# Optimization experiments

Measured on AMD Instinct MI355X. Metric: run time of the kernel, lower is better.

## Reference

```python
import jax, jax.numpy as jnp
import numpy as np
from jax.scipy.ndimage import map_coordinates

B, G, C, H, W = 8, 16, 1, 384, 384
K = 3                    # rectangular (box) kernel size
KV = float(K * K)        # kernel volume (sum of ones kernel)
LBD = 1.0
SMOOTH_DR = 1e-5         # monai LNCC default smooth_dr (smooth_nr = 0)


def setup_inputs() -> dict:
    key = jax.random.key(0)
    k1, k2 = jax.random.split(key)
    images = jax.random.normal(k1, (B, G, C, H, W), dtype=jnp.float32)
    warps = jax.random.normal(k2, (B, G, 2, H, W), dtype=jnp.float32)
    return {"images": images, "warps": warps}


def _warp2d(images, flow):
    """Bilinear warp. images [N,C,H,W], flow [N,2,H,W] (pixel displacements,
    channel 0 = x/width, channel 1 = y/height). Border-clamped sampling."""
    gy, gx = jnp.meshgrid(jnp.arange(H, dtype=images.dtype),
                          jnp.arange(W, dtype=images.dtype), indexing="ij")
    cy = gy[None] + flow[:, 1]   # [N,H,W]
    cx = gx[None] + flow[:, 0]   # [N,H,W]

    def samp(img2d, cy_, cx_):
        return map_coordinates(img2d, [cy_, cx_], order=1, mode="nearest")

    # vmap over channels, then over batch
    per_img = jax.vmap(samp, in_axes=(0, None, None))        # over C
    return jax.vmap(per_img, in_axes=(0, 0, 0))(images, cy, cx)  # over N


def _box_sum(x):
    """3x3 box-filter sum with zero padding (SAME). x: [N,C,H,W]."""
    k = jnp.ones((1, 1, K, K), x.dtype)
    return jax.lax.conv_general_dilated(
        x, k, window_strides=(1, 1), padding="SAME",
        dimension_numbers=("NCHW", "OIHW", "NCHW"))


def _lncc_loss(pred, target):
    """monai LocalNormalizedCrossCorrelationLoss (rectangular kernel)."""
    t_sum = _box_sum(target)
    p_sum = _box_sum(pred)
    t2_sum = _box_sum(target * target)
    p2_sum = _box_sum(pred * pred)
    tp_sum = _box_sum(target * pred)
    t_avg = t_sum / KV
    p_avg = p_sum / KV
    cross = tp_sum - p_avg * t_sum
    t_var = jnp.maximum(t2_sum - t_avg * t_sum, 0.0)
    p_var = jnp.maximum(p2_sum - p_avg * p_sum, 0.0)
    ncc = (cross * cross) / (t_var * p_var + SMOOTH_DR)
    return -jnp.mean(ncc)


def reference(images, warps):
    imgs = images.reshape(B * G, C, H, W)
    flow = warps.reshape(B * G, 2, H, W)
    warped = _warp2d(imgs, flow)                       # [B*G,C,H,W]
    template = jnp.mean(warped, axis=0, keepdims=True)  # [1,C,H,W]
    lncc = _lncc_loss(jnp.broadcast_to(template, warped.shape), warped)
    # Grad2d('l2') on warps [B,G,2,H,W]
    dy = warps[:, :, :, 1:, :] - warps[:, :, :, :-1, :]
    dx = warps[:, :, :, :, 1:] - warps[:, :, :, :, :-1]
    g2 = (jnp.mean(dx * dx) + jnp.mean(dy * dy)) / 2.0
    return lncc + LBD * g2
```

## Files before the change

### kernel.cpp

```cpp
#include <hip/hip_runtime.h>
#include <hip/hip_fp16.h>

#define HH 384
#define WW 384
#define HW (HH * WW)
#define NIMG 128
#define NPIX (NIMG * HW)
#define GRAD_CNT 37650432.0

#define K1_TH 8
#define K1_M  3
#define K1_NT (HH / K1_TH)
#define K1_SROWS (K1_TH + 2 * K1_M)
#define K1_LS 428
#define NP_G (K1_NT * NIMG)

#define K2_SPLIT 4

#define K3_T 32
#define K3_NX (WW / K3_T)
#define K3_TILES (K3_NX * (HH / K3_T))
#define NP_N (K3_TILES * NIMG)

__device__ inline int skew_off(int x) {
    int g = x >> 2;
    return 4 * (g + (g >> 3)) + (x & 3);
}

__device__ inline void block_reduce_store_256(float v, float* dst) {
    #pragma unroll
    for (int o = 32; o > 0; o >>= 1) v += __shfl_down(v, o);
    __shared__ float s[4];
    int wave = threadIdx.x >> 6, lane = threadIdx.x & 63;
    if (lane == 0) s[wave] = v;
    __syncthreads();
    if (threadIdx.x == 0) *dst = s[0] + s[1] + s[2] + s[3];
}

__global__ __launch_bounds__(256, 6) void warp_grad_kernel(
        const float* __restrict__ images, const float* __restrict__ warps,
        __half* __restrict__ warped, float* __restrict__ partialsG) {
    __shared__ float simg[K1_SROWS * K1_LS];
    int n = blockIdx.y;
    int yt = blockIdx.x;
    int y0 = yt * K1_TH;
    int ys0 = max(0, y0 - K1_M);
    int ys1 = min(HH - 1, y0 + K1_TH - 1 + K1_M);
    int cnt = ys1 - ys0 + 1;
    const float* img = images + (size_t)n * HW;
    int tid = threadIdx.x;

    for (int i = tid; i < cnt * 96; i += 256) {
        int r = i / 96, gg = i - r * 96;
        float4 v = *(const float4*)(img + (ys0 + r) * WW + gg * 4);
        *(float4*)(simg + r * K1_LS + 4 * (gg + (gg >> 3))) = v;
    }
    __syncthreads();

    const float* flow0 = warps + (size_t)n * 2 * HW;
    const float* flow1 = flow0 + HW;
    float g = 0.f;

    #pragma unroll
    for (int gi = 0; gi < 3; ++gi) {
        int p4 = gi * 256 + tid;
        int r = p4 / 96;
        int c4 = p4 - r * 96;
        int x0 = c4 * 4;
        int y = y0 + r;
        int base = y * WW + x0;

        float4 f0 = *(const float4*)(flow0 + base);
        float4 f1 = *(const float4*)(flow1 + base);

        float d;
        d = f0.y - f0.x; g += d * d;  d = f1.y - f1.x; g += d * d;
        d = f0.z - f0.y; g += d * d;  d = f1.z - f1.y; g += d * d;
        d = f0.w - f0.z; g += d * d;  d = f1.w - f1.z; g += d * d;
        if (x0 + 4 < WW) {
            float a0 = flow0[base + 4], a1 = flow1[base + 4];
            d = a0 - f0.w; g += d * d;  d = a1 - f1.w; g += d * d;
        }
        if (y + 1 < HH) {
            float4 b0 = *(const float4*)(flow0 + base + WW);
            float4 b1 = *(const float4*)(flow1 + base + WW);
            d = b0.x - f0.x; g += d * d;  d = b1.x - f1.x; g += d * d;
            d = b0.y - f0.y; g += d * d;  d = b1.y - f1.y; g += d * d;
            d = b0.z - f0.z; g += d * d;  d = b1.z - f1.z; g += d * d;
            d = b0.w - f0.w; g += d * d;  d = b1.w - f1.w; g += d * d;
        }

        float fxa[4] = {f0.x, f0.y, f0.z, f0.w};
        float fya[4] = {f1.x, f1.y, f1.z, f1.w};
        float o[4];
        #pragma unroll
        for (int j = 0; j < 4; ++j) {
            float cx = (float)(x0 + j) + fxa[j];
            float cy = (float)y + fya[j];
            float flx = floorf(cx), fly = floorf(cy);
            float wx = cx - flx, wy = cy - fly;
            int xi = (int)flx, yi = (int)fly;
            int x0c = min(max(xi, 0), WW - 1), x1c = min(max(xi + 1, 0), WW - 1);
            int y0c = min(max(yi, 0), HH - 1), y1c = min(max(yi + 1, 0), HH - 1);
            float v00, v01, v10, v11;
            if (y0c >= ys0 && y1c <= ys1) {
                const float* r0 = simg + (y0c - ys0) * K1_LS;
                const float* r1 = simg + (y1c - ys0) * K1_LS;
                int oa = skew_off(x0c), ob = skew_off(x1c);
                v00 = r0[oa]; v01 = r0[ob];
                v10 = r1[oa]; v11 = r1[ob];
            } else {
                v00 = img[y0c * WW + x0c]; v01 = img[y0c * WW + x1c];
                v10 = img[y1c * WW + x0c]; v11 = img[y1c * WW + x1c];
            }
            float top = v00 + wx * (v01 - v00);
            float bot = v10 + wx * (v11 - v10);
            o[j] = top + wy * (bot - top);
        }
        union { __half2 h2[2]; uint2 u; } cv;
        cv.h2[0] = __floats2half2_rn(o[0], o[1]);
        cv.h2[1] = __floats2half2_rn(o[2], o[3]);
        *(uint2*)(warped + (size_t)n * HW + base) = cv.u;
    }
    block_reduce_store_256(g, &partialsG[(size_t)n * K1_NT + yt]);
}

__global__ __launch_bounds__(256) void template_part_kernel(
        const __half* __restrict__ warped, float* __restrict__ tpart) {
    int p4 = blockIdx.x * 256 + threadIdx.x;
    int q = blockIdx.y;
    const __half* p = warped + (size_t)q * (NIMG / K2_SPLIT) * HW + p4 * 4;
    float4 s = {0.f, 0.f, 0.f, 0.f};
    #pragma unroll 8
    for (int nn = 0; nn < NIMG / K2_SPLIT; ++nn) {
        union { uint2 u; __half2 h2[2]; } cv;
        cv.u = *(const uint2*)(p + (size_t)nn * HW);
        float2 lo = __half22float2(cv.h2[0]);
        float2 hi = __half22float2(cv.h2[1]);
        s.x += lo.x; s.y += lo.y; s.z += hi.x; s.w += hi.y;
    }
    *(float4*)(tpart + (size_t)q * HW + p4 * 4) = s;
}

__global__ __launch_bounds__(256) void lncc_kernel(
        const __half* __restrict__ warped, const float* __restrict__ tpart,
        float* __restrict__ partialsN) {
    __shared__ float st[34][40];
    __shared__ float sp[34][40];
    int n = blockIdx.y;
    int tile = blockIdx.x;
    int tyt = tile / K3_NX, txt = tile - tyt * K3_NX;
    int oy0 = tyt * K3_T, ox0 = txt * K3_T;
    const __half* t = warped + (size_t)n * HW;
    int tid = threadIdx.x;
    const float invN = 1.f / (float)NIMG;

    for (int i = tid; i < 34 * 10; i += 256) {
        int ly = i / 10, c = i - (i / 10) * 10;
        int gy = oy0 + ly - 1;
        int gx = ox0 - 4 + c * 4;
        float4 tv = {0.f, 0.f, 0.f, 0.f}, pv = {0.f, 0.f, 0.f, 0.f};
        if (gy >= 0 && gy < HH && gx >= 0 && gx + 3 < WW) {
            union { uint2 u; __half2 h2[2]; } cv;
            cv.u = *(const uint2*)(t + gy * WW + gx);
            float2 lo = __half22float2(cv.h2[0]);
            float2 hi = __half22float2(cv.h2[1]);
            tv = make_float4(lo.x, lo.y, hi.x, hi.y);
            const float* q = tpart + gy * WW + gx;
            float4 a = *(const float4*)q;
            float4 b = *(const float4*)(q + HW);
            float4 c2 = *(const float4*)(q + 2 * HW);
            float4 e = *(const float4*)(q + 3 * HW);
            pv = make_float4((a.x + b.x + c2.x + e.x) * invN,
                             (a.y + b.y + c2.y + e.y) * invN,
                             (a.z + b.z + c2.z + e.z) * invN,
                             (a.w + b.w + c2.w + e.w) * invN);
        }
        *(float4*)&st[ly][c * 4] = tv;
        *(float4*)&sp[ly][c * 4] = pv;
    }
    __syncthreads();

    int tx = tid & 7, ty = tid >> 3;
    int xb = tx * 4;
    float cT[6] = {0,0,0,0,0,0}, cP[6] = {0,0,0,0,0,0};
    float cT2[6] = {0,0,0,0,0,0}, cP2[6] = {0,0,0,0,0,0}, cTP[6] = {0,0,0,0,0,0};
    #pragma unroll
    for (int r = 0; r < 3; ++r) {
        float t0 = st[ty + r][xb + 3];
        float4 t4 = *(const float4*)&st[ty + r][xb + 4];
        float t5 = st[ty + r][xb + 8];
        float p0 = sp[ty + r][xb + 3];
        float4 p4 = *(const float4*)&sp[ty + r][xb + 4];
        float p5 = sp[ty + r][xb + 8];
        float tv[6] = {t0, t4.x, t4.y, t4.z, t4.w, t5};
        float pv[6] = {p0, p4.x, p4.y, p4.z, p4.w, p5};
        #pragma unroll
        for (int c = 0; c < 6; ++c) {
            cT[c] += tv[c]; cP[c] += pv[c];
            cT2[c] = fmaf(tv[c], tv[c], cT2[c]);
            cP2[c] = fmaf(pv[c], pv[c], cP2[c]);
            cTP[c] = fmaf(tv[c], pv[c], cTP[c]);
        }
    }
    const float inv9 = 1.f / 9.f;
    float nccsum = 0.f;
    #pragma unroll
    for (int j = 0; j < 4; ++j) {
        float ts = cT[j] + cT[j + 1] + cT[j + 2];
        float ps = cP[j] + cP[j + 1] + cP[j + 2];
        float t2s = cT2[j] + cT2[j + 1] + cT2[j + 2];
        float p2s = cP2[j] + cP2[j + 1] + cP2[j + 2];
        float tps = cTP[j] + cTP[j + 1] + cTP[j + 2];
        float cross = tps - (ps * inv9) * ts;
        float tvar = fmaxf(t2s - (ts * inv9) * ts, 0.f);
        float pvar = fmaxf(p2s - (ps * inv9) * ps, 0.f);
        nccsum += (cross * cross) / (tvar * pvar + 1e-5f);
    }
    block_reduce_store_256(nccsum, &partialsN[(size_t)n * K3_TILES + tile]);
}

__global__ __launch_bounds__(1024) void finalize_kernel(
        const float* __restrict__ pN, const float* __restrict__ pG,
        float* __restrict__ out) {
    double accN = 0.0, accG = 0.0;
    for (int i = threadIdx.x; i < NP_N; i += 1024) accN += (double)pN[i];
    for (int i = threadIdx.x; i < NP_G; i += 1024) accG += (double)pG[i];
    #pragma unroll
    for (int o = 32; o > 0; o >>= 1) {
        accN += __shfl_down(accN, o);
        accG += __shfl_down(accG, o);
    }
    __shared__ double sN[16], sG[16];
    int wave = threadIdx.x >> 6, lane = threadIdx.x & 63;
    if (lane == 0) { sN[wave] = accN; sG[wave] = accG; }
    __syncthreads();
    if (threadIdx.x == 0) {
        double tN = 0.0, tG = 0.0;
        #pragma unroll
        for (int w = 0; w < 16; ++w) { tN += sN[w]; tG += sG[w]; }
        double lncc = -(tN / (double)NPIX);
        double g2 = tG / (2.0 * GRAD_CNT);
        out[0] = (float)(lncc + g2);
    }
}

extern "C" void kernel_launch(void* const* d_in, const int* in_sizes, int n_in,
                              void* d_out, int out_size, void* d_ws, size_t ws_size,
                              hipStream_t stream) {
    const float* images = (const float*)d_in[0];
    const float* warps  = (const float*)d_in[1];
    float* out = (float*)d_out;

    __half* warped  = (__half*)d_ws;
    float* fbase    = (float*)((char*)d_ws + (size_t)NPIX * 2);
    float* partialsN = fbase;
    float* partialsG = partialsN + NP_N;
    float* tpart     = partialsG + NP_G;

    warp_grad_kernel<<<dim3(K1_NT, NIMG), dim3(256), 0, stream>>>(
        images, warps, warped, partialsG);
    template_part_kernel<<<dim3(HW / 4 / 256, K2_SPLIT), dim3(256), 0, stream>>>(
        warped, tpart);
    lncc_kernel<<<dim3(K3_TILES, NIMG), dim3(256), 0, stream>>>(
        warped, tpart, partialsN);
    finalize_kernel<<<dim3(1), dim3(1024), 0, stream>>>(
        partialsN, partialsG, out);
}
```

Measured before the change: 131.8 us.

## Store warp source tile as fp16 in LDS and widen template split

New measurement: 151.3 us. 14.8% more time.

```diff
diff --git a/kernel.cpp b/kernel.cpp
--- a/kernel.cpp
+++ b/kernel.cpp
@@ -9,23 +9,20 @@
 #define GRAD_CNT 37650432.0
 
 #define K1_TH 8
-#define K1_M  3
+#define K1_M  4
 #define K1_NT (HH / K1_TH)
 #define K1_SROWS (K1_TH + 2 * K1_M)
-#define K1_LS 428
+#define K1_LSH 432
 #define NP_G (K1_NT * NIMG)
 
-#define K2_SPLIT 4
+#define K2_SPLIT 8
 
 #define K3_T 32
 #define K3_NX (WW / K3_T)
 #define K3_TILES (K3_NX * (HH / K3_T))
 #define NP_N (K3_TILES * NIMG)
 
-__device__ inline int skew_off(int x) {
-    int g = x >> 2;
-    return 4 * (g + (g >> 3)) + (x & 3);
-}
+__device__ inline int pad_off(int x) { return x + 4 * (x >> 5); }
 
 __device__ inline void block_reduce_store_256(float v, float* dst) {
     #pragma unroll
@@ -37,10 +34,10 @@
     if (threadIdx.x == 0) *dst = s[0] + s[1] + s[2] + s[3];
 }
 
-__global__ __launch_bounds__(256, 6) void warp_grad_kernel(
+__global__ __launch_bounds__(256, 8) void warp_grad_kernel(
         const float* __restrict__ images, const float* __restrict__ warps,
         __half* __restrict__ warped, float* __restrict__ partialsG) {
-    __shared__ float simg[K1_SROWS * K1_LS];
+    __shared__ __half simg[K1_SROWS * K1_LSH];
     int n = blockIdx.y;
     int yt = blockIdx.x;
     int y0 = yt * K1_TH;
@@ -52,8 +49,12 @@
 
     for (int i = tid; i < cnt * 96; i += 256) {
         int r = i / 96, gg = i - r * 96;
-        float4 v = *(const float4*)(img + (ys0 + r) * WW + gg * 4);
-        *(float4*)(simg + r * K1_LS + 4 * (gg + (gg >> 3))) = v;
+        int x0 = gg * 4;
+        float4 v = *(const float4*)(img + (ys0 + r) * WW + x0);
+        union { __half2 h2[2]; uint2 u; } pk;
+        pk.h2[0] = __floats2half2_rn(v.x, v.y);
+        pk.h2[1] = __floats2half2_rn(v.z, v.w);
+        *(uint2*)(simg + r * K1_LSH + pad_off(x0)) = pk.u;
     }
     __syncthreads();
 
@@ -104,11 +105,11 @@
             int y0c = min(max(yi, 0), HH - 1), y1c = min(max(yi + 1, 0), HH - 1);
             float v00, v01, v10, v11;
             if (y0c >= ys0 && y1c <= ys1) {
-                const float* r0 = simg + (y0c - ys0) * K1_LS;
-                const float* r1 = simg + (y1c - ys0) * K1_LS;
-                int oa = skew_off(x0c), ob = skew_off(x1c);
-                v00 = r0[oa]; v01 = r0[ob];
-                v10 = r1[oa]; v11 = r1[ob];
+                const __half* r0 = simg + (y0c - ys0) * K1_LSH;
+                const __half* r1 = simg + (y1c - ys0) * K1_LSH;
+                int oa = pad_off(x0c), ob = pad_off(x1c);
+                v00 = __half2float(r0[oa]); v01 = __half2float(r0[ob]);
+                v10 = __half2float(r1[oa]); v11 = __half2float(r1[ob]);
             } else {
                 v00 = img[y0c * WW + x0c]; v01 = img[y0c * WW + x1c];
                 v10 = img[y1c * WW + x0c]; v11 = img[y1c * WW + x1c];
@@ -167,14 +168,13 @@
             float2 hi = __half22float2(cv.h2[1]);
             tv = make_float4(lo.x, lo.y, hi.x, hi.y);
             const float* q = tpart + gy * WW + gx;
-            float4 a = *(const float4*)q;
-            float4 b = *(const float4*)(q + HW);
-            float4 c2 = *(const float4*)(q + 2 * HW);
-            float4 e = *(const float4*)(q + 3 * HW);
-            pv = make_float4((a.x + b.x + c2.x + e.x) * invN,
-                             (a.y + b.y + c2.y + e.y) * invN,
-                             (a.z + b.z + c2.z + e.z) * invN,
-                             (a.w + b.w + c2.w + e.w) * invN);
+            float sx = 0, sy = 0, sz = 0, sw = 0;
+            #pragma unroll
+            for (int pl = 0; pl < K2_SPLIT; ++pl) {
+                float4 a = *(const float4*)(q + (size_t)pl * HW);
+                sx += a.x; sy += a.y; sz += a.z; sw += a.w;
+            }
+            pv = make_float4(sx * invN, sy * invN, sz * invN, sw * invN);
         }
         *(float4*)&st[ly][c * 4] = tv;
         *(float4*)&sp[ly][c * 4] = pv;
```
